# Optimization experiments

Hardware: AMD Instinct MI355X
Metric: run time of the kernel (lower is better)

Reference implementation:

```python
import jax, jax.numpy as jnp
import numpy as np

N_NODES = 50000
N_EDGES = 640000
D = 128


def setup_inputs() -> dict:
    key = jax.random.key(0)
    ks = jax.random.split(key, 8)
    nfeats = jax.random.normal(ks[0], (N_NODES, 1, D), dtype=jnp.float32)
    efeats = jax.random.normal(ks[1], (N_EDGES, 1, D), dtype=jnp.float32)
    # Linear params (PyTorch convention: weight [out, in])
    W_msg_w = jax.random.normal(ks[2], (D, 2 * D), dtype=jnp.float32) * 0.05
    W_msg_b = jax.random.normal(ks[3], (D,), dtype=jnp.float32) * 0.05
    W_apply_w = jax.random.normal(ks[4], (D, 2 * D), dtype=jnp.float32) * 0.05
    W_apply_b = jax.random.normal(ks[5], (D,), dtype=jnp.float32) * 0.05
    src = jax.random.randint(ks[6], (N_EDGES,), 0, N_NODES, dtype=jnp.int32)
    dst = jax.random.randint(ks[7], (N_EDGES,), 0, N_NODES, dtype=jnp.int32)
    return {
        "nfeats": nfeats, "efeats": efeats,
        "W_msg_w": W_msg_w, "W_msg_b": W_msg_b,
        "W_apply_w": W_apply_w, "W_apply_b": W_apply_b,
        "src": src, "dst": dst,
    }


def reference(nfeats, efeats, W_msg_w, W_msg_b, W_apply_w, W_apply_b, src, dst):
    n_nodes = nfeats.shape[0]
    # message: W_msg(cat[src_h, edge_h])  -> [E, 1, D_out]
    msg_in = jnp.concatenate([nfeats[src], efeats], axis=-1)  # [E,1,2D]
    m = jnp.einsum("eqi,oi->eqo", msg_in, W_msg_w) + W_msg_b
    # segment-mean over destination nodes (DGL fn.mean; zero for isolated nodes)
    sums = jax.ops.segment_sum(m, dst, num_segments=n_nodes)  # [N,1,D]
    counts = jax.ops.segment_sum(jnp.ones((m.shape[0],), m.dtype), dst,
                                 num_segments=n_nodes)  # [N]
    h_neigh = sums / jnp.maximum(counts, 1.0)[:, None, None]
    # apply: relu(W_apply(cat[h, h_neigh]))
    upd_in = jnp.concatenate([nfeats, h_neigh], axis=-1)  # [N,1,2D]
    out = jax.nn.relu(jnp.einsum("nqi,oi->nqo", upd_in, W_apply_w) + W_apply_b)
    return out
```

## Files before the change

kernel.cpp:

```cpp
#include <hip/hip_runtime.h>

#define D 128
#define TWO_D 256
#define LDSR 264

typedef __attribute__((ext_vector_type(4))) float f32x4;
typedef __attribute__((ext_vector_type(8))) short bf16x8;

static __device__ __forceinline__ unsigned short f2bf(float x) {
  union { float f; unsigned u; } v; v.f = x;
  unsigned r = (v.u + 0x7fffu + ((v.u >> 16) & 1u)) >> 16;
  return (unsigned short)r;
}

__global__ void prep_pack(const float* __restrict__ wmsg,
                          const float* __restrict__ wapp,
                          unsigned short* __restrict__ Wp,
                          int* __restrict__ counts, int n_nodes) {
  int p = blockIdx.x * blockDim.x + threadIdx.x;
  int j = p & 7;
  int lane = (p >> 3) & 63;
  int ot = (p >> 9) & 7;
  int k0i = (p >> 12) & 7;
  int g = p >> 15;
  int o = ot * 16 + (lane & 15);
  int k = k0i * 32 + (lane >> 4) * 8 + j;
  const float* W = g ? wapp : wmsg;
  Wp[p] = f2bf(W[o * 256 + k]);
  if (p < n_nodes) counts[p] = 0;
}

__global__ void hist_rank_kernel(const int* __restrict__ dst, int* __restrict__ counts,
                                 int* __restrict__ rank, int n_edges) {
  int e = blockIdx.x * blockDim.x + threadIdx.x;
  if (e < n_edges) rank[e] = atomicAdd(&counts[dst[e]], 1);
}

__global__ void scan_part(const int* __restrict__ counts, int* __restrict__ partial,
                          int n) {
  __shared__ int lds[256];
  int b = blockIdx.x, t = threadIdx.x;
  int g0 = b * 1024 + t * 4;
  int s = 0;
  #pragma unroll
  for (int j = 0; j < 4; ++j) { int g = g0 + j; if (g < n) s += counts[g]; }
  lds[t] = s;
  __syncthreads();
  for (int off = 128; off > 0; off >>= 1) {
    if (t < off) lds[t] += lds[t + off];
    __syncthreads();
  }
  if (t == 0) partial[b] = lds[0];
}

__global__ void scan_write(const int* __restrict__ counts, const int* __restrict__ partial,
                           int* __restrict__ offsets, int n, int n_edges, int nb) {
  __shared__ int lds[256];
  __shared__ int pb[64];
  int b = blockIdx.x, t = threadIdx.x;
  if (t < nb) pb[t] = partial[t];
  __syncthreads();
  int base = 0;
  for (int k = 0; k < b; ++k) base += pb[k];
  int g0 = b * 1024 + t * 4;
  int c0 = (g0 + 0 < n) ? counts[g0 + 0] : 0;
  int c1 = (g0 + 1 < n) ? counts[g0 + 1] : 0;
  int c2 = (g0 + 2 < n) ? counts[g0 + 2] : 0;
  int c3 = (g0 + 3 < n) ? counts[g0 + 3] : 0;
  lds[t] = c0 + c1 + c2 + c3;
  __syncthreads();
  for (int off = 1; off < 256; off <<= 1) {
    int v = (t >= off) ? lds[t - off] : 0;
    __syncthreads();
    lds[t] += v;
    __syncthreads();
  }
  int texc = base + ((t > 0) ? lds[t - 1] : 0);
  if (g0 + 0 < n) offsets[g0 + 0] = texc;
  if (g0 + 1 < n) offsets[g0 + 1] = texc + c0;
  if (g0 + 2 < n) offsets[g0 + 2] = texc + c0 + c1;
  if (g0 + 3 < n) offsets[g0 + 3] = texc + c0 + c1 + c2;
  if (b == 0 && t == 0) offsets[n] = n_edges;
}

__global__ void scatter_kernel(const int* __restrict__ dst, const int* __restrict__ src,
                               const int* __restrict__ rank,
                               const int* __restrict__ offsets,
                               int2* __restrict__ edge_list, int n_edges) {
  int e = blockIdx.x * blockDim.x + threadIdx.x;
  if (e < n_edges) {
    int d = dst[e];
    edge_list[offsets[d] + rank[e]] = make_int2(e, src[e]);
  }
}

__global__ __launch_bounds__(256) void gather_kernel(
    const float* __restrict__ nfeats, const float* __restrict__ efeats,
    const int2* __restrict__ edge_list, const int* __restrict__ offsets,
    unsigned short* __restrict__ X1, int n_nodes) {
  int w = (blockIdx.x * 256 + threadIdx.x) >> 6;
  int lane = threadIdx.x & 63;
  if (w >= n_nodes) return;
  int beg = offsets[w], end = offsets[w + 1];
  int cnt = end - beg;
  const f32x4* nf4 = (const f32x4*)nfeats;
  const f32x4* ef4 = (const f32x4*)efeats;
  const int c32 = lane & 31;
  const int slot = lane >> 5;
  f32x4 accn = (f32x4){0.f, 0.f, 0.f, 0.f};
  f32x4 acce = (f32x4){0.f, 0.f, 0.f, 0.f};

  for (int j0 = beg; j0 < end; j0 += 64) {
    int nj = end - j0; if (nj > 64) nj = 64;
    int e = 0, s = 0;
    if (lane < nj) { int2 es = edge_list[j0 + lane]; e = es.x; s = es.y; }
    int i0 = slot, i1 = 2 + slot;
    int ee0 = __shfl(e, i0), ss0 = __shfl(s, i0);
    int ee1 = __shfl(e, i1), ss1 = __shfl(s, i1);
    bool v0 = i0 < nj, v1 = i1 < nj;
    f32x4 a0 = (f32x4){0.f,0.f,0.f,0.f}, b0 = a0, a1 = a0, b1v = a0;
    if (v0) { a0 = nf4[(size_t)ss0 * 32 + c32];
              b0 = __builtin_nontemporal_load(&ef4[(size_t)ee0 * 32 + c32]); }
    if (v1) { a1 = nf4[(size_t)ss1 * 32 + c32];
              b1v = __builtin_nontemporal_load(&ef4[(size_t)ee1 * 32 + c32]); }
    for (int p = 0; p < nj; p += 4) {
      int n0 = (p + 4 + slot) & 63, n1 = (p + 6 + slot) & 63;
      int eeN0 = __shfl(e, n0), ssN0 = __shfl(s, n0);
      int eeN1 = __shfl(e, n1), ssN1 = __shfl(s, n1);
      bool w0 = p + 4 + slot < nj, w1 = p + 6 + slot < nj;
      f32x4 aN0 = (f32x4){0.f,0.f,0.f,0.f}, bN0 = aN0, aN1 = aN0, bN1 = aN0;
      if (w0) { aN0 = nf4[(size_t)ssN0 * 32 + c32];
                bN0 = __builtin_nontemporal_load(&ef4[(size_t)eeN0 * 32 + c32]); }
      if (w1) { aN1 = nf4[(size_t)ssN1 * 32 + c32];
                bN1 = __builtin_nontemporal_load(&ef4[(size_t)eeN1 * 32 + c32]); }
      if (v0) { accn += a0; acce += b0; }
      if (v1) { accn += a1; acce += b1v; }
      a0 = aN0; b0 = bN0; a1 = aN1; b1v = bN1; v0 = w0; v1 = w1;
    }
  }
  #pragma unroll
  for (int k = 0; k < 4; ++k) {
    accn[k] += __shfl_xor(accn[k], 32);
    acce[k] += __shfl_xor(acce[k], 32);
  }
  float inv = (cnt > 0) ? 1.0f / (float)cnt : 0.0f;
  f32x4 v = (lane < 32) ? accn : acce;
  ushort4 o;
  o.x = f2bf(v[0] * inv); o.y = f2bf(v[1] * inv);
  o.z = f2bf(v[2] * inv); o.w = f2bf(v[3] * inv);
  ((ushort4*)(X1 + (size_t)w * TWO_D))[lane] = o;
}

__global__ __launch_bounds__(256) void node_gemm(
    const unsigned short* __restrict__ X1,
    const unsigned short* __restrict__ Wp,
    const float* __restrict__ b1,
    const float* __restrict__ b2,
    const float* __restrict__ nfeats,
    const int* __restrict__ offsets,
    float* __restrict__ out,
    int n_nodes) {
  __shared__ unsigned short xt[64 * LDSR];
  __shared__ int cnts[64];
  const int tid = threadIdx.x;
  const int base = blockIdx.x * 64;

  if (tid < 64) {
    int g = base + tid;
    cnts[tid] = (g < n_nodes) ? (offsets[g + 1] - offsets[g]) : 0;
  }
  #pragma unroll
  for (int it = 0; it < 8; ++it) {
    int chunk = tid + it * 256;
    int r = chunk >> 5, c = chunk & 31;
    int g = base + r;
    uint4 v = make_uint4(0, 0, 0, 0);
    if (g < n_nodes) v = ((const uint4*)X1)[(size_t)g * 32 + c];
    *(uint4*)&xt[r * LDSR + c * 8] = v;
  }
  __syncthreads();

  const int lane = tid & 63;
  const int wid = tid >> 6;
  const int m16 = lane & 15;
  const int quad = lane >> 4;
  const int arow = wid * 16 + m16;
  const int lane8 = lane << 3;

  f32x4 acc[8];
  #pragma unroll
  for (int ot = 0; ot < 8; ++ot) acc[ot] = (f32x4){0.f, 0.f, 0.f, 0.f};

  #pragma unroll
  for (int k0i = 0; k0i < 8; ++k0i) {
    bf16x8 a = *(const bf16x8*)&xt[arow * LDSR + k0i * 32 + quad * 8];
    #pragma unroll
    for (int ot = 0; ot < 8; ++ot) {
      bf16x8 b = *(const bf16x8*)&Wp[((k0i * 8 + ot) << 9) + lane8];
      acc[ot] = __builtin_amdgcn_mfma_f32_16x16x32_bf16(a, b, acc[ot], 0, 0, 0);
    }
  }
  __syncthreads();

  #pragma unroll
  for (int ot = 0; ot < 8; ++ot) {
    int o = ot * 16 + m16;
    float bias = b1[o];
    #pragma unroll
    for (int r = 0; r < 4; ++r) {
      int m = wid * 16 + quad * 4 + r;
      float h = acc[ot][r] + (cnts[m] > 0 ? bias : 0.0f);
      xt[m * LDSR + 128 + o] = f2bf(h);
    }
  }
  #pragma unroll
  for (int it = 0; it < 8; ++it) {
    int chunk = tid + it * 256;
    int r = chunk >> 5, c = chunk & 31;
    int g = base + r;
    float4 v = make_float4(0.f, 0.f, 0.f, 0.f);
    if (g < n_nodes) v = ((const float4*)nfeats)[(size_t)g * 32 + c];
    ushort4 bv;
    bv.x = f2bf(v.x); bv.y = f2bf(v.y); bv.z = f2bf(v.z); bv.w = f2bf(v.w);
    *(ushort4*)&xt[r * LDSR + c * 4] = bv;
  }
  __syncthreads();

  #pragma unroll
  for (int ot = 0; ot < 8; ++ot) acc[ot] = (f32x4){0.f, 0.f, 0.f, 0.f};

  #pragma unroll
  for (int k0i = 0; k0i < 8; ++k0i) {
    bf16x8 a = *(const bf16x8*)&xt[arow * LDSR + k0i * 32 + quad * 8];
    #pragma unroll
    for (int ot = 0; ot < 8; ++ot) {
      bf16x8 b = *(const bf16x8*)&Wp[32768 + ((k0i * 8 + ot) << 9) + lane8];
      acc[ot] = __builtin_amdgcn_mfma_f32_16x16x32_bf16(a, b, acc[ot], 0, 0, 0);
    }
  }
  #pragma unroll
  for (int ot = 0; ot < 8; ++ot) {
    int o = ot * 16 + m16;
    float bias = b2[o];
    #pragma unroll
    for (int r = 0; r < 4; ++r) {
      int m = wid * 16 + quad * 4 + r;
      int g = base + m;
      if (g < n_nodes) {
        float v = acc[ot][r] + bias;
        out[(size_t)g * D + o] = v > 0.f ? v : 0.f;
      }
    }
  }
}

extern "C" void kernel_launch(void* const* d_in, const int* in_sizes, int n_in,
                              void* d_out, int out_size, void* d_ws, size_t ws_size,
                              hipStream_t stream) {
  const float* nfeats = (const float*)d_in[0];
  const float* efeats = (const float*)d_in[1];
  const float* Wmsg_f = (const float*)d_in[2];
  const float* b1     = (const float*)d_in[3];
  const float* Wapp_f = (const float*)d_in[4];
  const float* b2     = (const float*)d_in[5];
  const int*   src    = (const int*)d_in[6];
  const int*   dst    = (const int*)d_in[7];
  const int n_nodes = in_sizes[0] / D;
  const int n_edges = in_sizes[6];
  const int nb = (n_nodes + 1023) / 1024;

  char* ws = (char*)d_ws;
  size_t off = 0;
  unsigned short* X1 = (unsigned short*)(ws + off); off += (size_t)n_nodes * TWO_D * 2;
  unsigned short* Wp = (unsigned short*)(ws + off); off += (size_t)2 * D * TWO_D * 2;
  int* counts    = (int*)(ws + off); off += (size_t)n_nodes * 4;
  int* offsets   = (int*)(ws + off); off += (size_t)(n_nodes + 1) * 4;
  int* rank      = (int*)(ws + off); off += (size_t)n_edges * 4;
  int* partial   = (int*)(ws + off); off += 64 * 4;
  int2* edge_list = (int2*)(ws + off); off += (size_t)n_edges * 8;
  (void)ws_size; (void)n_in; (void)out_size;

  prep_pack<<<256, 256, 0, stream>>>(Wmsg_f, Wapp_f, Wp, counts, n_nodes);
  hist_rank_kernel<<<(n_edges + 255) / 256, 256, 0, stream>>>(dst, counts, rank, n_edges);
  scan_part<<<nb, 256, 0, stream>>>(counts, partial, n_nodes);
  scan_write<<<nb, 256, 0, stream>>>(counts, partial, offsets, n_nodes, n_edges, nb);
  scatter_kernel<<<(n_edges + 255) / 256, 256, 0, stream>>>(dst, src, rank, offsets, edge_list, n_edges);
  gather_kernel<<<(n_nodes + 3) / 4, 256, 0, stream>>>(nfeats, efeats, edge_list, offsets, X1, n_nodes);
  node_gemm<<<(n_nodes + 63) / 64, 256, 0, stream>>>(X1, Wp, b1, b2, nfeats, offsets, (float*)d_out, n_nodes);
}
```

Before: 558.0 us.

## Fuse all stages into one persistent kernel with global barriers

```diff
diff --git a/kernel.cpp b/kernel.cpp
--- a/kernel.cpp
+++ b/kernel.cpp
@@ -13,244 +13,230 @@
   return (unsigned short)r;
 }
 
-__global__ void prep_pack(const float* __restrict__ wmsg,
-                          const float* __restrict__ wapp,
-                          unsigned short* __restrict__ Wp,
-                          int* __restrict__ counts, int n_nodes) {
-  int p = blockIdx.x * blockDim.x + threadIdx.x;
-  int j = p & 7;
-  int lane = (p >> 3) & 63;
-  int ot = (p >> 9) & 7;
-  int k0i = (p >> 12) & 7;
-  int g = p >> 15;
-  int o = ot * 16 + (lane & 15);
-  int k = k0i * 32 + (lane >> 4) * 8 + j;
-  const float* W = g ? wapp : wmsg;
-  Wp[p] = f2bf(W[o * 256 + k]);
-  if (p < n_nodes) counts[p] = 0;
-}
-
-__global__ void hist_rank_kernel(const int* __restrict__ dst, int* __restrict__ counts,
-                                 int* __restrict__ rank, int n_edges) {
-  int e = blockIdx.x * blockDim.x + threadIdx.x;
-  if (e < n_edges) rank[e] = atomicAdd(&counts[dst[e]], 1);
-}
-
-__global__ void scan_part(const int* __restrict__ counts, int* __restrict__ partial,
-                          int n) {
-  __shared__ int lds[256];
-  int b = blockIdx.x, t = threadIdx.x;
-  int g0 = b * 1024 + t * 4;
-  int s = 0;
-  #pragma unroll
-  for (int j = 0; j < 4; ++j) { int g = g0 + j; if (g < n) s += counts[g]; }
-  lds[t] = s;
+static __device__ __forceinline__ void gbar(int* bar, int target) {
   __syncthreads();
-  for (int off = 128; off > 0; off >>= 1) {
-    if (t < off) lds[t] += lds[t + off];
-    __syncthreads();
-  }
-  if (t == 0) partial[b] = lds[0];
-}
-
-__global__ void scan_write(const int* __restrict__ counts, const int* __restrict__ partial,
-                           int* __restrict__ offsets, int n, int n_edges, int nb) {
-  __shared__ int lds[256];
-  __shared__ int pb[64];
-  int b = blockIdx.x, t = threadIdx.x;
-  if (t < nb) pb[t] = partial[t];
+  if (threadIdx.x == 0) {
+    __hip_atomic_fetch_add(bar, 1, __ATOMIC_ACQ_REL, __HIP_MEMORY_SCOPE_AGENT);
+    long long t0 = clock64();
+    while (__hip_atomic_load(bar, __ATOMIC_ACQUIRE, __HIP_MEMORY_SCOPE_AGENT) < target) {
+      __builtin_amdgcn_s_sleep(2);
+      if ((clock64() - t0) > 400000000LL) break;
+    }
+  }
   __syncthreads();
-  int base = 0;
-  for (int k = 0; k < b; ++k) base += pb[k];
-  int g0 = b * 1024 + t * 4;
-  int c0 = (g0 + 0 < n) ? counts[g0 + 0] : 0;
-  int c1 = (g0 + 1 < n) ? counts[g0 + 1] : 0;
-  int c2 = (g0 + 2 < n) ? counts[g0 + 2] : 0;
-  int c3 = (g0 + 3 < n) ? counts[g0 + 3] : 0;
-  lds[t] = c0 + c1 + c2 + c3;
-  __syncthreads();
-  for (int off = 1; off < 256; off <<= 1) {
-    int v = (t >= off) ? lds[t - off] : 0;
-    __syncthreads();
-    lds[t] += v;
-    __syncthreads();
-  }
-  int texc = base + ((t > 0) ? lds[t - 1] : 0);
-  if (g0 + 0 < n) offsets[g0 + 0] = texc;
-  if (g0 + 1 < n) offsets[g0 + 1] = texc + c0;
-  if (g0 + 2 < n) offsets[g0 + 2] = texc + c0 + c1;
-  if (g0 + 3 < n) offsets[g0 + 3] = texc + c0 + c1 + c2;
-  if (b == 0 && t == 0) offsets[n] = n_edges;
-}
-
-__global__ void scatter_kernel(const int* __restrict__ dst, const int* __restrict__ src,
-                               const int* __restrict__ rank,
-                               const int* __restrict__ offsets,
-                               int2* __restrict__ edge_list, int n_edges) {
-  int e = blockIdx.x * blockDim.x + threadIdx.x;
-  if (e < n_edges) {
-    int d = dst[e];
-    edge_list[offsets[d] + rank[e]] = make_int2(e, src[e]);
-  }
-}
-
-__global__ __launch_bounds__(256) void gather_kernel(
+}
+
+__global__ __launch_bounds__(256, 4) void gcn_fused(
     const float* __restrict__ nfeats, const float* __restrict__ efeats,
-    const int2* __restrict__ edge_list, const int* __restrict__ offsets,
-    unsigned short* __restrict__ X1, int n_nodes) {
-  int w = (blockIdx.x * 256 + threadIdx.x) >> 6;
-  int lane = threadIdx.x & 63;
-  if (w >= n_nodes) return;
-  int beg = offsets[w], end = offsets[w + 1];
-  int cnt = end - beg;
-  const f32x4* nf4 = (const f32x4*)nfeats;
-  const f32x4* ef4 = (const f32x4*)efeats;
-  const int c32 = lane & 31;
-  const int slot = lane >> 5;
-  f32x4 accn = (f32x4){0.f, 0.f, 0.f, 0.f};
-  f32x4 acce = (f32x4){0.f, 0.f, 0.f, 0.f};
-
-  for (int j0 = beg; j0 < end; j0 += 64) {
-    int nj = end - j0; if (nj > 64) nj = 64;
-    int e = 0, s = 0;
-    if (lane < nj) { int2 es = edge_list[j0 + lane]; e = es.x; s = es.y; }
-    int i0 = slot, i1 = 2 + slot;
-    int ee0 = __shfl(e, i0), ss0 = __shfl(s, i0);
-    int ee1 = __shfl(e, i1), ss1 = __shfl(s, i1);
-    bool v0 = i0 < nj, v1 = i1 < nj;
-    f32x4 a0 = (f32x4){0.f,0.f,0.f,0.f}, b0 = a0, a1 = a0, b1v = a0;
-    if (v0) { a0 = nf4[(size_t)ss0 * 32 + c32];
-              b0 = __builtin_nontemporal_load(&ef4[(size_t)ee0 * 32 + c32]); }
-    if (v1) { a1 = nf4[(size_t)ss1 * 32 + c32];
-              b1v = __builtin_nontemporal_load(&ef4[(size_t)ee1 * 32 + c32]); }
-    for (int p = 0; p < nj; p += 4) {
-      int n0 = (p + 4 + slot) & 63, n1 = (p + 6 + slot) & 63;
-      int eeN0 = __shfl(e, n0), ssN0 = __shfl(s, n0);
-      int eeN1 = __shfl(e, n1), ssN1 = __shfl(s, n1);
-      bool w0 = p + 4 + slot < nj, w1 = p + 6 + slot < nj;
-      f32x4 aN0 = (f32x4){0.f,0.f,0.f,0.f}, bN0 = aN0, aN1 = aN0, bN1 = aN0;
-      if (w0) { aN0 = nf4[(size_t)ssN0 * 32 + c32];
-                bN0 = __builtin_nontemporal_load(&ef4[(size_t)eeN0 * 32 + c32]); }
-      if (w1) { aN1 = nf4[(size_t)ssN1 * 32 + c32];
-                bN1 = __builtin_nontemporal_load(&ef4[(size_t)eeN1 * 32 + c32]); }
-      if (v0) { accn += a0; acce += b0; }
-      if (v1) { accn += a1; acce += b1v; }
-      a0 = aN0; b0 = bN0; a1 = aN1; b1v = bN1; v0 = w0; v1 = w1;
-    }
-  }
-  #pragma unroll
-  for (int k = 0; k < 4; ++k) {
-    accn[k] += __shfl_xor(accn[k], 32);
-    acce[k] += __shfl_xor(acce[k], 32);
-  }
-  float inv = (cnt > 0) ? 1.0f / (float)cnt : 0.0f;
-  f32x4 v = (lane < 32) ? accn : acce;
-  ushort4 o;
-  o.x = f2bf(v[0] * inv); o.y = f2bf(v[1] * inv);
-  o.z = f2bf(v[2] * inv); o.w = f2bf(v[3] * inv);
-  ((ushort4*)(X1 + (size_t)w * TWO_D))[lane] = o;
-}
-
-__global__ __launch_bounds__(256) void node_gemm(
-    const unsigned short* __restrict__ X1,
-    const unsigned short* __restrict__ Wp,
-    const float* __restrict__ b1,
-    const float* __restrict__ b2,
-    const float* __restrict__ nfeats,
-    const int* __restrict__ offsets,
-    float* __restrict__ out,
-    int n_nodes) {
+    const float* __restrict__ wmsg, const float* __restrict__ b1,
+    const float* __restrict__ wapp, const float* __restrict__ b2,
+    const int* __restrict__ src, const int* __restrict__ dst,
+    unsigned short* __restrict__ X1, unsigned short* __restrict__ Wp,
+    int* __restrict__ d_counts, int* __restrict__ offsets,
+    int* __restrict__ rank, int2* __restrict__ edge_list,
+    int* __restrict__ bar,
+    float* __restrict__ out, int n_nodes, int n_edges) {
   __shared__ unsigned short xt[64 * LDSR];
   __shared__ int cnts[64];
+  __shared__ int sc[256];
+
   const int tid = threadIdx.x;
-  const int base = blockIdx.x * 64;
-
-  if (tid < 64) {
-    int g = base + tid;
-    cnts[tid] = (g < n_nodes) ? (offsets[g + 1] - offsets[g]) : 0;
-  }
-  #pragma unroll
-  for (int it = 0; it < 8; ++it) {
-    int chunk = tid + it * 256;
-    int r = chunk >> 5, c = chunk & 31;
-    int g = base + r;
-    uint4 v = make_uint4(0, 0, 0, 0);
-    if (g < n_nodes) v = ((const uint4*)X1)[(size_t)g * 32 + c];
-    *(uint4*)&xt[r * LDSR + c * 8] = v;
-  }
-  __syncthreads();
-
-  const int lane = tid & 63;
-  const int wid = tid >> 6;
-  const int m16 = lane & 15;
-  const int quad = lane >> 4;
-  const int arow = wid * 16 + m16;
-  const int lane8 = lane << 3;
-
-  f32x4 acc[8];
-  #pragma unroll
-  for (int ot = 0; ot < 8; ++ot) acc[ot] = (f32x4){0.f, 0.f, 0.f, 0.f};
-
-  #pragma unroll
-  for (int k0i = 0; k0i < 8; ++k0i) {
-    bf16x8 a = *(const bf16x8*)&xt[arow * LDSR + k0i * 32 + quad * 8];
+  const int bid = blockIdx.x;
+  const int GS = gridDim.x;
+  const int nthr = GS * 256;
+  const int gtid = bid * 256 + tid;
+
+  for (int p = gtid; p < 65536; p += nthr) {
+    int j = p & 7;
+    int lane = (p >> 3) & 63;
+    int ot = (p >> 9) & 7;
+    int k0i = (p >> 12) & 7;
+    int g = p >> 15;
+    int o = ot * 16 + (lane & 15);
+    int k = k0i * 32 + (lane >> 4) * 8 + j;
+    const float* W = g ? wapp : wmsg;
+    Wp[p] = f2bf(W[o * 256 + k]);
+  }
+  for (int p = gtid; p < n_nodes; p += nthr) d_counts[p] = 0;
+  gbar(bar, GS);
+
+  for (int e = gtid; e < n_edges; e += nthr)
+    rank[e] = atomicAdd(&d_counts[dst[e]], 1);
+  gbar(bar, 2 * GS);
+
+  if (bid == 0) {
+    const int C = (n_nodes + 255) / 256;
+    int lo = tid * C, hi = lo + C;
+    if (lo > n_nodes) lo = n_nodes;
+    if (hi > n_nodes) hi = n_nodes;
+    int s = 0;
+    for (int i = lo; i < hi; ++i) s += d_counts[i];
+    sc[tid] = s;
+    __syncthreads();
+    for (int off = 1; off < 256; off <<= 1) {
+      int v = (tid >= off) ? sc[tid - off] : 0;
+      __syncthreads();
+      sc[tid] += v;
+      __syncthreads();
+    }
+    int base = (tid > 0) ? sc[tid - 1] : 0;
+    for (int i = lo; i < hi; ++i) { int c = d_counts[i]; offsets[i] = base; base += c; }
+    if (tid == 0) offsets[n_nodes] = n_edges;
+  }
+  gbar(bar, 3 * GS);
+
+  for (int e = gtid; e < n_edges; e += nthr) {
+    int d2 = dst[e];
+    edge_list[offsets[d2] + rank[e]] = make_int2(e, src[e]);
+  }
+  gbar(bar, 4 * GS);
+
+  {
+    const int lane = tid & 63;
+    const int nwaves = nthr >> 6;
+    const f32x4* nf4 = (const f32x4*)nfeats;
+    const f32x4* ef4 = (const f32x4*)efeats;
+    const int c32 = lane & 31;
+    const int slot = lane >> 5;
+    for (int w = (gtid >> 6); w < n_nodes; w += nwaves) {
+      int beg = offsets[w], end = offsets[w + 1];
+      int cnt = end - beg;
+      f32x4 accn = (f32x4){0.f, 0.f, 0.f, 0.f};
+      f32x4 acce = (f32x4){0.f, 0.f, 0.f, 0.f};
+      for (int j0 = beg; j0 < end; j0 += 64) {
+        int njj = end - j0; if (njj > 64) njj = 64;
+        int e = 0, s = 0;
+        if (lane < njj) { int2 es = edge_list[j0 + lane]; e = es.x; s = es.y; }
+        int i0 = slot, i1 = 2 + slot;
+        int ee0 = __shfl(e, i0), ss0 = __shfl(s, i0);
+        int ee1 = __shfl(e, i1), ss1 = __shfl(s, i1);
+        bool v0 = i0 < njj, v1 = i1 < njj;
+        f32x4 a0 = (f32x4){0.f,0.f,0.f,0.f}, b0 = a0, a1 = a0, b1v = a0;
+        if (v0) { a0 = nf4[(size_t)ss0 * 32 + c32];
+                  b0 = __builtin_nontemporal_load(&ef4[(size_t)ee0 * 32 + c32]); }
+        if (v1) { a1 = nf4[(size_t)ss1 * 32 + c32];
+                  b1v = __builtin_nontemporal_load(&ef4[(size_t)ee1 * 32 + c32]); }
+        for (int p = 0; p < njj; p += 4) {
+          int n0 = (p + 4 + slot) & 63, n1 = (p + 6 + slot) & 63;
+          int eeN0 = __shfl(e, n0), ssN0 = __shfl(s, n0);
+          int eeN1 = __shfl(e, n1), ssN1 = __shfl(s, n1);
+          bool u0 = p + 4 + slot < njj, u1 = p + 6 + slot < njj;
+          f32x4 aN0 = (f32x4){0.f,0.f,0.f,0.f}, bN0 = aN0, aN1 = aN0, bN1 = aN0;
+          if (u0) { aN0 = nf4[(size_t)ssN0 * 32 + c32];
+                    bN0 = __builtin_nontemporal_load(&ef4[(size_t)eeN0 * 32 + c32]); }
+          if (u1) { aN1 = nf4[(size_t)ssN1 * 32 + c32];
+                    bN1 = __builtin_nontemporal_load(&ef4[(size_t)eeN1 * 32 + c32]); }
+          if (v0) { accn += a0; acce += b0; }
+          if (v1) { accn += a1; acce += b1v; }
+          a0 = aN0; b0 = bN0; a1 = aN1; b1v = bN1; v0 = u0; v1 = u1;
+        }
+      }
+      #pragma unroll
+      for (int k = 0; k < 4; ++k) {
+        accn[k] += __shfl_xor(accn[k], 32);
+        acce[k] += __shfl_xor(acce[k], 32);
+      }
+      float inv = (cnt > 0) ? 1.0f / (float)cnt : 0.0f;
+      f32x4 vv = (lane < 32) ? accn : acce;
+      ushort4 o4;
+      o4.x = f2bf(vv[0] * inv); o4.y = f2bf(vv[1] * inv);
+      o4.z = f2bf(vv[2] * inv); o4.w = f2bf(vv[3] * inv);
+      ((ushort4*)(X1 + (size_t)w * TWO_D))[lane] = o4;
+    }
+  }
+  gbar(bar, 5 * GS);
+
+  const int nblk = (n_nodes + 63) / 64;
+  for (int blk = bid; blk < nblk; blk += GS) {
+    const int base = blk * 64;
+    if (tid < 64) {
+      int g = base + tid;
+      cnts[tid] = (g < n_nodes) ? (offsets[g + 1] - offsets[g]) : 0;
+    }
+    #pragma unroll
+    for (int it = 0; it < 8; ++it) {
+      int chunk = tid + it * 256;
+      int r = chunk >> 5, c = chunk & 31;
+      int g = base + r;
+      uint4 v = make_uint4(0, 0, 0, 0);
+      if (g < n_nodes) v = ((const uint4*)X1)[(size_t)g * 32 + c];
+      *(uint4*)&xt[r * LDSR + c * 8] = v;
+    }
+    __syncthreads();
+
+    const int lane = tid & 63;
+    const int wid = tid >> 6;
+    const int m16 = lane & 15;
+    const int quad = lane >> 4;
+    const int arow = wid * 16 + m16;
+    const int lane8 = lane << 3;
+
+    f32x4 acc[8];
+    #pragma unroll
+    for (int ot = 0; ot < 8; ++ot) acc[ot] = (f32x4){0.f, 0.f, 0.f, 0.f};
+
+    #pragma unroll
+    for (int k0i = 0; k0i < 8; ++k0i) {
+      bf16x8 a = *(const bf16x8*)&xt[arow * LDSR + k0i * 32 + quad * 8];
+      #pragma unroll
+      for (int ot = 0; ot < 8; ++ot) {
+        bf16x8 b = *(const bf16x8*)&Wp[((k0i * 8 + ot) << 9) + lane8];
+        acc[ot] = __builtin_amdgcn_mfma_f32_16x16x32_bf16(a, b, acc[ot], 0, 0, 0);
+      }
+    }
+    __syncthreads();
+
     #pragma unroll
     for (int ot = 0; ot < 8; ++ot) {
-      bf16x8 b = *(const bf16x8*)&Wp[((k0i * 8 + ot) << 9) + lane8];
-      acc[ot] = __builtin_amdgcn_mfma_f32_16x16x32_bf16(a, b, acc[ot], 0, 0, 0);
-    }
-  }
-  __syncthreads();
-
-  #pragma unroll
-  for (int ot = 0; ot < 8; ++ot) {
-    int o = ot * 16 + m16;
-    float bias = b1[o];
-    #pragma unroll
-    for (int r = 0; r < 4; ++r) {
-      int m = wid * 16 + quad * 4 + r;
-      float h = acc[ot][r] + (cnts[m] > 0 ? bias : 0.0f);
-      xt[m * LDSR + 128 + o] = f2bf(h);
-    }
-  }
-  #pragma unroll
-  for (int it = 0; it < 8; ++it) {
-    int chunk = tid + it * 256;
-    int r = chunk >> 5, c = chunk & 31;
-    int g = base + r;
-    float4 v = make_float4(0.f, 0.f, 0.f, 0.f);
-    if (g < n_nodes) v = ((const float4*)nfeats)[(size_t)g * 32 + c];
-    ushort4 bv;
-    bv.x = f2bf(v.x); bv.y = f2bf(v.y); bv.z = f2bf(v.z); bv.w = f2bf(v.w);
-    *(ushort4*)&xt[r * LDSR + c * 4] = bv;
-  }
-  __syncthreads();
-
-  #pragma unroll
-  for (int ot = 0; ot < 8; ++ot) acc[ot] = (f32x4){0.f, 0.f, 0.f, 0.f};
-
-  #pragma unroll
-  for (int k0i = 0; k0i < 8; ++k0i) {
-    bf16x8 a = *(const bf16x8*)&xt[arow * LDSR + k0i * 32 + quad * 8];
+      int o = ot * 16 + m16;
+      float bias = b1[o];
+      #pragma unroll
+      for (int r = 0; r < 4; ++r) {
+        int m = wid * 16 + quad * 4 + r;
+        float h = acc[ot][r] + (cnts[m] > 0 ? bias : 0.0f);
+        xt[m * LDSR + 128 + o] = f2bf(h);
+      }
+    }
+    #pragma unroll
+    for (int it = 0; it < 8; ++it) {
+      int chunk = tid + it * 256;
+      int r = chunk >> 5, c = chunk & 31;
+      int g = base + r;
+      float4 v = make_float4(0.f, 0.f, 0.f, 0.f);
+      if (g < n_nodes) v = ((const float4*)nfeats)[(size_t)g * 32 + c];
+      ushort4 bv;
+      bv.x = f2bf(v.x); bv.y = f2bf(v.y); bv.z = f2bf(v.z); bv.w = f2bf(v.w);
+      *(ushort4*)&xt[r * LDSR + c * 4] = bv;
+    }
+    __syncthreads();
+
+    #pragma unroll
+    for (int ot = 0; ot < 8; ++ot) acc[ot] = (f32x4){0.f, 0.f, 0.f, 0.f};
+
+    #pragma unroll
+    for (int k0i = 0; k0i < 8; ++k0i) {
+      bf16x8 a = *(const bf16x8*)&xt[arow * LDSR + k0i * 32 + quad * 8];
+      #pragma unroll
+      for (int ot = 0; ot < 8; ++ot) {
+        bf16x8 b = *(const bf16x8*)&Wp[32768 + ((k0i * 8 + ot) << 9) + lane8];
+        acc[ot] = __builtin_amdgcn_mfma_f32_16x16x32_bf16(a, b, acc[ot], 0, 0, 0);
+      }
+    }
     #pragma unroll
     for (int ot = 0; ot < 8; ++ot) {
-      bf16x8 b = *(const bf16x8*)&Wp[32768 + ((k0i * 8 + ot) << 9) + lane8];
-      acc[ot] = __builtin_amdgcn_mfma_f32_16x16x32_bf16(a, b, acc[ot], 0, 0, 0);
-    }
-  }
-  #pragma unroll
-  for (int ot = 0; ot < 8; ++ot) {
-    int o = ot * 16 + m16;
-    float bias = b2[o];
-    #pragma unroll
-    for (int r = 0; r < 4; ++r) {
-      int m = wid * 16 + quad * 4 + r;
-      int g = base + m;
-      if (g < n_nodes) {
-        float v = acc[ot][r] + bias;
-        out[(size_t)g * D + o] = v > 0.f ? v : 0.f;
-      }
-    }
+      int o = ot * 16 + m16;
+      float bias = b2[o];
+      #pragma unroll
+      for (int r = 0; r < 4; ++r) {
+        int m = wid * 16 + quad * 4 + r;
+        int g = base + m;
+        if (g < n_nodes) {
+          float v = acc[ot][r] + bias;
+          out[(size_t)g * D + o] = v > 0.f ? v : 0.f;
+        }
+      }
+    }
+    __syncthreads();
   }
 }
 
@@ -267,7 +253,6 @@
   const int*   dst    = (const int*)d_in[7];
   const int n_nodes = in_sizes[0] / D;
   const int n_edges = in_sizes[6];
-  const int nb = (n_nodes + 1023) / 1024;
 
   char* ws = (char*)d_ws;
   size_t off = 0;
@@ -276,15 +261,27 @@
   int* counts    = (int*)(ws + off); off += (size_t)n_nodes * 4;
   int* offsets   = (int*)(ws + off); off += (size_t)(n_nodes + 1) * 4;
   int* rank      = (int*)(ws + off); off += (size_t)n_edges * 4;
-  int* partial   = (int*)(ws + off); off += 64 * 4;
   int2* edge_list = (int2*)(ws + off); off += (size_t)n_edges * 8;
+  int* bar       = (int*)(ws + off); off += 64;
   (void)ws_size; (void)n_in; (void)out_size;
 
-  prep_pack<<<256, 256, 0, stream>>>(Wmsg_f, Wapp_f, Wp, counts, n_nodes);
-  hist_rank_kernel<<<(n_edges + 255) / 256, 256, 0, stream>>>(dst, counts, rank, n_edges);
-  scan_part<<<nb, 256, 0, stream>>>(counts, partial, n_nodes);
-  scan_write<<<nb, 256, 0, stream>>>(counts, partial, offsets, n_nodes, n_edges, nb);
-  scatter_kernel<<<(n_edges + 255) / 256, 256, 0, stream>>>(dst, src, rank, offsets, edge_list, n_edges);
-  gather_kernel<<<(n_nodes + 3) / 4, 256, 0, stream>>>(nfeats, efeats, edge_list, offsets, X1, n_nodes);
-  node_gemm<<<(n_nodes + 63) / 64, 256, 0, stream>>>(X1, Wp, b1, b2, nfeats, offsets, (float*)d_out, n_nodes);
-}
+  static int G = 0;
+  if (G == 0) {
+    int bpc = 0;
+    if (hipOccupancyMaxActiveBlocksPerMultiprocessor(&bpc, gcn_fused, 256, 0) != hipSuccess || bpc < 1)
+      bpc = 1;
+    int dev = 0;
+    hipGetDevice(&dev);
+    int ncu = 0;
+    if (hipDeviceGetAttribute(&ncu, hipDeviceAttributeMultiprocessorCount, dev) != hipSuccess || ncu < 1)
+      ncu = 256;
+    long g = (long)bpc * (long)ncu;
+    if (g > 4096) g = 4096;
+    G = (int)g;
+  }
+
+  hipMemsetAsync(bar, 0, sizeof(int), stream);
+  gcn_fused<<<G, 256, 0, stream>>>(nfeats, efeats, Wmsg_f, b1, Wapp_f, b2, src, dst,
+                                   X1, Wp, counts, offsets, rank, edge_list, bar,
+                                   (float*)d_out, n_nodes, n_edges);
+}
```

Result: slower. 2.213 ms (+296.7%).

## Fuse neighbor gather into node GEMM and merge weight packing with histogram

Applied to the files above, without the earlier changes.

```diff
diff --git a/kernel.cpp b/kernel.cpp
--- a/kernel.cpp
+++ b/kernel.cpp
@@ -13,27 +13,25 @@
   return (unsigned short)r;
 }
 
-__global__ void prep_pack(const float* __restrict__ wmsg,
+__global__ void prep_hist(const float* __restrict__ wmsg,
                           const float* __restrict__ wapp,
                           unsigned short* __restrict__ Wp,
-                          int* __restrict__ counts, int n_nodes) {
+                          const int* __restrict__ dst,
+                          int* __restrict__ counts, int* __restrict__ rank,
+                          int n_edges) {
   int p = blockIdx.x * blockDim.x + threadIdx.x;
-  int j = p & 7;
-  int lane = (p >> 3) & 63;
-  int ot = (p >> 9) & 7;
-  int k0i = (p >> 12) & 7;
-  int g = p >> 15;
-  int o = ot * 16 + (lane & 15);
-  int k = k0i * 32 + (lane >> 4) * 8 + j;
-  const float* W = g ? wapp : wmsg;
-  Wp[p] = f2bf(W[o * 256 + k]);
-  if (p < n_nodes) counts[p] = 0;
-}
-
-__global__ void hist_rank_kernel(const int* __restrict__ dst, int* __restrict__ counts,
-                                 int* __restrict__ rank, int n_edges) {
-  int e = blockIdx.x * blockDim.x + threadIdx.x;
-  if (e < n_edges) rank[e] = atomicAdd(&counts[dst[e]], 1);
+  if (p < 65536) {
+    int j = p & 7;
+    int lane = (p >> 3) & 63;
+    int ot = (p >> 9) & 7;
+    int k0i = (p >> 12) & 7;
+    int g = p >> 15;
+    int o = ot * 16 + (lane & 15);
+    int k = k0i * 32 + (lane >> 4) * 8 + j;
+    const float* W = g ? wapp : wmsg;
+    Wp[p] = f2bf(W[o * 256 + k]);
+  }
+  if (p < n_edges) rank[p] = atomicAdd(&counts[dst[p]], 1);
 }
 
 __global__ void scan_part(const int* __restrict__ counts, int* __restrict__ partial,
@@ -94,94 +92,76 @@
   }
 }
 
-__global__ __launch_bounds__(256) void gather_kernel(
+__global__ __launch_bounds__(256, 4) void gather_gemm(
     const float* __restrict__ nfeats, const float* __restrict__ efeats,
     const int2* __restrict__ edge_list, const int* __restrict__ offsets,
-    unsigned short* __restrict__ X1, int n_nodes) {
-  int w = (blockIdx.x * 256 + threadIdx.x) >> 6;
-  int lane = threadIdx.x & 63;
-  if (w >= n_nodes) return;
-  int beg = offsets[w], end = offsets[w + 1];
-  int cnt = end - beg;
-  const f32x4* nf4 = (const f32x4*)nfeats;
-  const f32x4* ef4 = (const f32x4*)efeats;
-  const int c32 = lane & 31;
-  const int slot = lane >> 5;
-  f32x4 accn = (f32x4){0.f, 0.f, 0.f, 0.f};
-  f32x4 acce = (f32x4){0.f, 0.f, 0.f, 0.f};
-
-  for (int j0 = beg; j0 < end; j0 += 64) {
-    int nj = end - j0; if (nj > 64) nj = 64;
-    int e = 0, s = 0;
-    if (lane < nj) { int2 es = edge_list[j0 + lane]; e = es.x; s = es.y; }
-    int i0 = slot, i1 = 2 + slot;
-    int ee0 = __shfl(e, i0), ss0 = __shfl(s, i0);
-    int ee1 = __shfl(e, i1), ss1 = __shfl(s, i1);
-    bool v0 = i0 < nj, v1 = i1 < nj;
-    f32x4 a0 = (f32x4){0.f,0.f,0.f,0.f}, b0 = a0, a1 = a0, b1v = a0;
-    if (v0) { a0 = nf4[(size_t)ss0 * 32 + c32];
-              b0 = __builtin_nontemporal_load(&ef4[(size_t)ee0 * 32 + c32]); }
-    if (v1) { a1 = nf4[(size_t)ss1 * 32 + c32];
-              b1v = __builtin_nontemporal_load(&ef4[(size_t)ee1 * 32 + c32]); }
-    for (int p = 0; p < nj; p += 4) {
-      int n0 = (p + 4 + slot) & 63, n1 = (p + 6 + slot) & 63;
-      int eeN0 = __shfl(e, n0), ssN0 = __shfl(s, n0);
-      int eeN1 = __shfl(e, n1), ssN1 = __shfl(s, n1);
-      bool w0 = p + 4 + slot < nj, w1 = p + 6 + slot < nj;
-      f32x4 aN0 = (f32x4){0.f,0.f,0.f,0.f}, bN0 = aN0, aN1 = aN0, bN1 = aN0;
-      if (w0) { aN0 = nf4[(size_t)ssN0 * 32 + c32];
-                bN0 = __builtin_nontemporal_load(&ef4[(size_t)eeN0 * 32 + c32]); }
-      if (w1) { aN1 = nf4[(size_t)ssN1 * 32 + c32];
-                bN1 = __builtin_nontemporal_load(&ef4[(size_t)eeN1 * 32 + c32]); }
-      if (v0) { accn += a0; acce += b0; }
-      if (v1) { accn += a1; acce += b1v; }
-      a0 = aN0; b0 = bN0; a1 = aN1; b1v = bN1; v0 = w0; v1 = w1;
-    }
-  }
-  #pragma unroll
-  for (int k = 0; k < 4; ++k) {
-    accn[k] += __shfl_xor(accn[k], 32);
-    acce[k] += __shfl_xor(acce[k], 32);
-  }
-  float inv = (cnt > 0) ? 1.0f / (float)cnt : 0.0f;
-  f32x4 v = (lane < 32) ? accn : acce;
-  ushort4 o;
-  o.x = f2bf(v[0] * inv); o.y = f2bf(v[1] * inv);
-  o.z = f2bf(v[2] * inv); o.w = f2bf(v[3] * inv);
-  ((ushort4*)(X1 + (size_t)w * TWO_D))[lane] = o;
-}
-
-__global__ __launch_bounds__(256) void node_gemm(
-    const unsigned short* __restrict__ X1,
     const unsigned short* __restrict__ Wp,
-    const float* __restrict__ b1,
-    const float* __restrict__ b2,
-    const float* __restrict__ nfeats,
-    const int* __restrict__ offsets,
-    float* __restrict__ out,
-    int n_nodes) {
+    const float* __restrict__ b1, const float* __restrict__ b2,
+    float* __restrict__ out, int n_nodes) {
   __shared__ unsigned short xt[64 * LDSR];
   __shared__ int cnts[64];
   const int tid = threadIdx.x;
   const int base = blockIdx.x * 64;
-
-  if (tid < 64) {
-    int g = base + tid;
-    cnts[tid] = (g < n_nodes) ? (offsets[g + 1] - offsets[g]) : 0;
-  }
-  #pragma unroll
-  for (int it = 0; it < 8; ++it) {
-    int chunk = tid + it * 256;
-    int r = chunk >> 5, c = chunk & 31;
-    int g = base + r;
-    uint4 v = make_uint4(0, 0, 0, 0);
-    if (g < n_nodes) v = ((const uint4*)X1)[(size_t)g * 32 + c];
-    *(uint4*)&xt[r * LDSR + c * 8] = v;
-  }
-  __syncthreads();
-
   const int lane = tid & 63;
   const int wid = tid >> 6;
+
+  {
+    const f32x4* nf4 = (const f32x4*)nfeats;
+    const f32x4* ef4 = (const f32x4*)efeats;
+    const int c32 = lane & 31;
+    const int slot = lane >> 5;
+    for (int i = 0; i < 16; ++i) {
+      const int row = wid * 16 + i;
+      const int w = base + row;
+      int beg = 0, end = 0;
+      if (w < n_nodes) { beg = offsets[w]; end = offsets[w + 1]; }
+      const int cnt = end - beg;
+      f32x4 accn = (f32x4){0.f, 0.f, 0.f, 0.f};
+      f32x4 acce = (f32x4){0.f, 0.f, 0.f, 0.f};
+      for (int j0 = beg; j0 < end; j0 += 64) {
+        int nj = end - j0; if (nj > 64) nj = 64;
+        int e = 0, s = 0;
+        if (lane < nj) { int2 es = edge_list[j0 + lane]; e = es.x; s = es.y; }
+        int i0 = slot, i1 = 2 + slot;
+        int ee0 = __shfl(e, i0), ss0 = __shfl(s, i0);
+        int ee1 = __shfl(e, i1), ss1 = __shfl(s, i1);
+        bool v0 = i0 < nj, v1 = i1 < nj;
+        f32x4 a0 = (f32x4){0.f,0.f,0.f,0.f}, b0 = a0, a1 = a0, b1v = a0;
+        if (v0) { a0 = nf4[(size_t)ss0 * 32 + c32];
+                  b0 = __builtin_nontemporal_load(&ef4[(size_t)ee0 * 32 + c32]); }
+        if (v1) { a1 = nf4[(size_t)ss1 * 32 + c32];
+                  b1v = __builtin_nontemporal_load(&ef4[(size_t)ee1 * 32 + c32]); }
+        for (int p = 0; p < nj; p += 4) {
+          int n0 = (p + 4 + slot) & 63, n1 = (p + 6 + slot) & 63;
+          int eeN0 = __shfl(e, n0), ssN0 = __shfl(s, n0);
+          int eeN1 = __shfl(e, n1), ssN1 = __shfl(s, n1);
+          bool u0 = p + 4 + slot < nj, u1 = p + 6 + slot < nj;
+          f32x4 aN0 = (f32x4){0.f,0.f,0.f,0.f}, bN0 = aN0, aN1 = aN0, bN1 = aN0;
+          if (u0) { aN0 = nf4[(size_t)ssN0 * 32 + c32];
+                    bN0 = __builtin_nontemporal_load(&ef4[(size_t)eeN0 * 32 + c32]); }
+          if (u1) { aN1 = nf4[(size_t)ssN1 * 32 + c32];
+                    bN1 = __builtin_nontemporal_load(&ef4[(size_t)eeN1 * 32 + c32]); }
+          if (v0) { accn += a0; acce += b0; }
+          if (v1) { accn += a1; acce += b1v; }
+          a0 = aN0; b0 = bN0; a1 = aN1; b1v = bN1; v0 = u0; v1 = u1;
+        }
+      }
+      #pragma unroll
+      for (int k = 0; k < 4; ++k) {
+        accn[k] += __shfl_xor(accn[k], 32);
+        acce[k] += __shfl_xor(acce[k], 32);
+      }
+      if (lane == 0) cnts[row] = cnt;
+      float inv = (cnt > 0) ? 1.0f / (float)cnt : 0.0f;
+      f32x4 vv = (lane < 32) ? accn : acce;
+      ushort4 o4;
+      o4.x = f2bf(vv[0] * inv); o4.y = f2bf(vv[1] * inv);
+      o4.z = f2bf(vv[2] * inv); o4.w = f2bf(vv[3] * inv);
+      *(ushort4*)&xt[row * LDSR + lane * 4] = o4;
+    }
+  }
+  __syncthreads();
+
   const int m16 = lane & 15;
   const int quad = lane >> 4;
   const int arow = wid * 16 + m16;
@@ -271,7 +251,6 @@
 
   char* ws = (char*)d_ws;
   size_t off = 0;
-  unsigned short* X1 = (unsigned short*)(ws + off); off += (size_t)n_nodes * TWO_D * 2;
   unsigned short* Wp = (unsigned short*)(ws + off); off += (size_t)2 * D * TWO_D * 2;
   int* counts    = (int*)(ws + off); off += (size_t)n_nodes * 4;
   int* offsets   = (int*)(ws + off); off += (size_t)(n_nodes + 1) * 4;
@@ -280,11 +259,14 @@
   int2* edge_list = (int2*)(ws + off); off += (size_t)n_edges * 8;
   (void)ws_size; (void)n_in; (void)out_size;
 
-  prep_pack<<<256, 256, 0, stream>>>(Wmsg_f, Wapp_f, Wp, counts, n_nodes);
-  hist_rank_kernel<<<(n_edges + 255) / 256, 256, 0, stream>>>(dst, counts, rank, n_edges);
+  hipMemsetAsync(counts, 0, (size_t)n_nodes * 4, stream);
+  prep_hist<<<(n_edges + 255) / 256, 256, 0, stream>>>(Wmsg_f, Wapp_f, Wp, dst,
+                                                       counts, rank, n_edges);
   scan_part<<<nb, 256, 0, stream>>>(counts, partial, n_nodes);
   scan_write<<<nb, 256, 0, stream>>>(counts, partial, offsets, n_nodes, n_edges, nb);
-  scatter_kernel<<<(n_edges + 255) / 256, 256, 0, stream>>>(dst, src, rank, offsets, edge_list, n_edges);
-  gather_kernel<<<(n_nodes + 3) / 4, 256, 0, stream>>>(nfeats, efeats, edge_list, offsets, X1, n_nodes);
-  node_gemm<<<(n_nodes + 63) / 64, 256, 0, stream>>>(X1, Wp, b1, b2, nfeats, offsets, (float*)d_out, n_nodes);
-}
+  scatter_kernel<<<(n_edges + 255) / 256, 256, 0, stream>>>(dst, src, rank, offsets,
+                                                            edge_list, n_edges);
+  gather_gemm<<<(n_nodes + 63) / 64, 256, 0, stream>>>(nfeats, efeats, edge_list,
+                                                       offsets, Wp, b1, b2,
+                                                       (float*)d_out, n_nodes);
+}
```

Result: no change. 552.3 us (-1.0%).
